# Performance work log

Measured on AMD Instinct MI355X. Metric: run time of the kernel, lower is better.

The kernel has to match this reference:

```python
import jax, jax.numpy as jnp
import numpy as np

T, B, C, H, W = 40, 256, 32, 8, 8
D = C * H * W  # 2048 flattened enc dim


def setup_inputs() -> dict:
    key = jax.random.key(0)
    k0, k1, k2 = jax.random.split(key, 3)
    x = jax.random.normal(k0, (T, B, C, H, W), dtype=jnp.float32)
    W0 = jax.random.normal(k1, (4 * C, 2 * C, 5, 5), dtype=jnp.float32) * 0.05
    b0 = jnp.zeros((4 * C,), dtype=jnp.float32)
    W1 = jax.random.normal(k2, (4 * C, 2 * C, 3, 3), dtype=jnp.float32) * 0.05
    b1 = jnp.zeros((4 * C,), dtype=jnp.float32)
    return {"x": x, "W0": W0, "b0": b0, "W1": W1, "b1": b1}


def _conv(x, w, b, pad):
    y = jax.lax.conv_general_dilated(
        x, w, window_strides=(1, 1), padding=[(pad, pad), (pad, pad)],
        dimension_numbers=("NCHW", "OIHW", "NCHW"))
    return y + b[None, :, None, None]


def _cell(inp, h, c, w, b, pad):
    # ConvLSTMCell: conv over concat(input, hidden) -> 4 gates
    g = _conv(jnp.concatenate([inp, h], axis=1), w, b, pad)
    i_g, f_g, o_g, c_g = jnp.split(g, 4, axis=1)
    c_new = jax.nn.sigmoid(f_g) * c + jax.nn.sigmoid(i_g) * jnp.tanh(c_g)
    h_new = jax.nn.sigmoid(o_g) * jnp.tanh(c_new)
    return h_new, c_new


def reference(x, W0, b0, W1, b1):
    Tn, Bn, Cn, Hn, Wn = x.shape
    Dn = Cn * Hn * Wn
    zeros = jnp.zeros((Bn, Cn, Hn, Wn), x.dtype)
    buf0 = jnp.zeros((Tn, Bn, Dn), x.dtype)  # growing prev_encs buffer, masked
    steps = jnp.arange(Tn)

    def body(carry, xt_t):
        xt, t = xt_t
        h0, c0, h1, c1, buf = carry
        h0, c0 = _cell(xt, h0, c0, W0, b0, 2)  # cell0: k=5, pad=2
        flat = h0.reshape(Bn, Dn)
        buf = buf.at[t].set(flat)
        # attention over encs[0..t] (softmax over a single entry at t=0 -> enc itself)
        dots = jnp.einsum("bd,tbd->bt", flat, buf)
        dots = jnp.where((steps <= t)[None, :], dots, -jnp.inf)
        wts = jax.nn.softmax(dots, axis=1)
        att = jnp.einsum("bt,tbd->bd", wts, buf).reshape(Bn, Cn, Hn, Wn)
        h1, c1 = _cell(att, h1, c1, W1, b1, 1)  # cell1: k=3, pad=1
        return (h0, c0, h1, c1, buf), h1

    _, ys = jax.lax.scan(body, (zeros, zeros, zeros, zeros, buf0), (x, steps))
    return ys  # [T, B, C, 8, 8]
```

## Files before the change

### kernel.cpp

```cpp
#include <hip/hip_runtime.h>

#define TT 40
#define NB 256
#define DD 2048
#define HISTL 28

typedef __bf16 bf16x8 __attribute__((ext_vector_type(8)));
typedef float f32x4 __attribute__((ext_vector_type(4)));
typedef unsigned short u16;
typedef unsigned int u32;
typedef u16 u16x8 __attribute__((ext_vector_type(8)));
typedef u16 u16x4 __attribute__((ext_vector_type(4)));

__device__ __forceinline__ u16 f2bf(float f) {
  u32 u = __builtin_bit_cast(u32, f);
  return (u16)((u + 0x7fffu + ((u >> 16) & 1u)) >> 16);
}
__device__ __forceinline__ float bf2f(u16 h) {
  return __builtin_bit_cast(float, ((u32)h) << 16);
}
__device__ __forceinline__ bf16x8 asbf(u16x8 v) { return __builtin_bit_cast(bf16x8, v); }

__device__ __forceinline__ float sigm(float x) { return 1.0f / (1.0f + __expf(-x)); }
__device__ __forceinline__ float tanh_(float x) {
  float e = __expf(-2.0f * fabsf(x));
  float t = (1.0f - e) / (1.0f + e);
  return copysignf(t, x);
}

__device__ __forceinline__ f32x4 mfma16(bf16x8 a, bf16x8 b, f32x4 c) {
  return __builtin_amdgcn_mfma_f32_16x16x32_bf16(a, b, c, 0, 0, 0);
}

__global__ void prep_weights(const float* __restrict__ W0, const float* __restrict__ W1,
                             u16* __restrict__ A0, u16* __restrict__ A1) {
  int tid = blockIdx.x * 256 + threadIdx.x;
  if (tid < 25600) {
    int lane = tid & 63;
    int kt = tid >> 9;
    int p = ((tid >> 6) & 7) * 16 + (lane & 15);
    int oc = (p & 3) * 32 + ((p >> 5) & 3) * 8 + ((p >> 4) & 1) * 4 + ((p >> 2) & 3);
    int kb = kt * 32 + (lane >> 4) * 8;
#pragma unroll
    for (int j = 0; j < 8; ++j) {
      int k = kb + j;
      int pos = k >> 6, ic = k & 63;
      int ky = pos / 5, kx = pos - ky * 5;
      A0[tid * 8 + j] = f2bf(W0[((oc * 64 + ic) * 5 + ky) * 5 + kx]);
    }
  } else if (tid < 25600 + 9216) {
    int t2 = tid - 25600;
    int lane = t2 & 63;
    int kt = t2 >> 9;
    int p = ((t2 >> 6) & 7) * 16 + (lane & 15);
    int oc = (p & 3) * 32 + ((p >> 5) & 3) * 8 + ((p >> 4) & 1) * 4 + ((p >> 2) & 3);
    int kb = kt * 32 + (lane >> 4) * 8;
#pragma unroll
    for (int j = 0; j < 8; ++j) {
      int k = kb + j;
      int pos = k >> 6, ic = k & 63;
      int ky = pos / 3, kx = pos - ky * 3;
      A1[t2 * 8 + j] = f2bf(W1[((oc * 64 + ic) * 3 + ky) * 3 + kx]);
    }
  }
}

template <int KK, int NKT, int SKB>
__device__ __forceinline__ void conv_loop(const u16* __restrict__ wsA, const u16* img,
                                          int w, int lane, f32x4 acc[4]) {
  const int ic0v = (lane >> 4) << 3;
  const int pb0 = ((lane & 15) >> 3) * 12 + (lane & 7);
  const bf16x8* A = (const bf16x8*)wsA;
  int aidx = w * 64 + lane;
  bf16x8 a0 = A[aidx];
  bf16x8 a1 = A[aidx + 512];
#pragma unroll
  for (int kt = 0; kt < NKT; ++kt) {
    bf16x8 nx = a1;
    if (kt + 2 < NKT) nx = A[aidx + 1024];
    const int pos = kt >> 1, ih = kt & 1;
    const int ky = pos / KK, kx = pos - ky * KK;
    const int Pb = pb0 + (ky * 12 + kx + SKB);
    const int idx = Pb * 64 + ((ic0v ^ ((Pb & 7) << 3)) ^ (ih << 5));
    u16x8 b0v = *(const u16x8*)(img + idx);
    u16x8 b1v = *(const u16x8*)(img + idx + 1536);
    u16x8 b2v = *(const u16x8*)(img + idx + 3072);
    u16x8 b3v = *(const u16x8*)(img + idx + 4608);
    acc[0] = mfma16(a0, asbf(b0v), acc[0]);
    acc[1] = mfma16(a0, asbf(b1v), acc[1]);
    acc[2] = mfma16(a0, asbf(b2v), acc[2]);
    acc[3] = mfma16(a0, asbf(b3v), acc[3]);
    a0 = a1;
    a1 = nx;
    aidx += 512;
  }
}

__device__ __forceinline__ int imin(int a, int b) { return a < b ? a : b; }

__global__ void __launch_bounds__(512, 1)
convlstm_main(const float* __restrict__ x, const float* __restrict__ b0g,
              const float* __restrict__ b1g, const u16* __restrict__ wsA0,
              const u16* __restrict__ wsA1, u16* __restrict__ buf,
              float* __restrict__ out) {
  alignas(16) __shared__ u16 imgA[9216];
  alignas(16) __shared__ u16 imgB[9216];
  alignas(16) __shared__ u16 hist[HISTL * DD];
  alignas(16) __shared__ u16 curr[DD];
  __shared__ float sdots[64];
  __shared__ float swts[64];

  const int tid = threadIdx.x;
  const int b = blockIdx.x;
  const int lane = tid & 63;
  const int w = tid >> 6;
  const int h = lane >> 4;
  const int l15 = lane & 15;

  for (int i = tid; i < 9216; i += 512) {
    imgA[i] = 0;
    imgB[i] = 0;
  }

  float c0st[4] = {};
  float c1st[4] = {};
  float bi0[4], bi1[4];
  const int ch = ((w >> 1) & 3) * 8 + (w & 1) * 4 + h;
#pragma unroll
  for (int j = 0; j < 4; ++j) {
    bi0[j] = b0g[j * 32 + ch];
    bi1[j] = b1g[j * 32 + ch];
  }

  const int Pldx = ((lane >> 3) + 2) * 12 + (lane & 7) + 2;
  const int swx = (Pldx & 7) << 3;
  const int Pl0 = ((l15 >> 3) + 2) * 12 + (l15 & 7) + 2;
  const int swh = (Pl0 & 7) << 3;
  const int e4 = tid * 4;
  const int chAtt = tid >> 4;
  const int pix0 = (tid & 15) * 4;
  const int PaB = ((pix0 >> 3) + 2) * 12 + (pix0 & 7) + 2;

  float xr[4];
  {
    const float* xp = x + (size_t)b * DD;
#pragma unroll
    for (int i = 0; i < 4; ++i) xr[i] = xp[(i * 8 + w) * 64 + lane];
  }

  __syncthreads();

  for (int t = 0; t < TT; ++t) {
#pragma unroll
    for (int i = 0; i < 4; ++i) {
      int c = i * 8 + w;
      imgA[Pldx * 64 + (c ^ swx)] = f2bf(xr[i]);
    }
    __syncthreads();

    if (t + 1 < TT) {
      const float* xp = x + (size_t)((t + 1) * NB + b) * DD;
#pragma unroll
      for (int i = 0; i < 4; ++i) xr[i] = xp[(i * 8 + w) * 64 + lane];
    }

    f32x4 acc[4];
    f32x4 zz = {0.f, 0.f, 0.f, 0.f};
#pragma unroll
    for (int nt = 0; nt < 4; ++nt) acc[nt] = zz;
    conv_loop<5, 50, 0>(wsA0, imgA, w, lane, acc);
    __syncthreads();

    u16* bufrow = buf + (size_t)(t * NB + b) * DD;
#pragma unroll
    for (int nt = 0; nt < 4; ++nt) {
      float ig = acc[nt][0] + bi0[0];
      float fg = acc[nt][1] + bi0[1];
      float og = acc[nt][2] + bi0[2];
      float cg = acc[nt][3] + bi0[3];
      float cn = sigm(fg) * c0st[nt] + sigm(ig) * tanh_(cg);
      float hn = sigm(og) * tanh_(cn);
      c0st[nt] = cn;
      u16 hb = f2bf(hn);
      imgA[(Pl0 + 24 * nt) * 64 + ((32 + ch) ^ swh)] = hb;
      int d = ch * 64 + nt * 16 + l15;
      curr[d] = hb;
      if (t < HISTL)
        hist[t * DD + d] = hb;
      else
        bufrow[d] = hb;
    }
    __syncthreads();

    {
      u16x8 fv[4];
      {
        const u16x8* rowT = (const u16x8*)curr;
#pragma unroll
        for (int i = 0; i < 4; ++i) fv[i] = rowT[i * 64 + lane];
      }
      int tp = w;
      for (; tp <= t && tp < HISTL; tp += 8) {
        const u16x8* rowP = (const u16x8*)&hist[tp * DD];
        u16x8 p0 = rowP[lane], p1 = rowP[64 + lane], p2 = rowP[128 + lane], p3 = rowP[192 + lane];
        float s0 = 0.f, s1 = 0.f, s2 = 0.f, s3 = 0.f;
#pragma unroll
        for (int j = 0; j < 8; ++j) {
          s0 += bf2f(fv[0][j]) * bf2f(p0[j]);
          s1 += bf2f(fv[1][j]) * bf2f(p1[j]);
          s2 += bf2f(fv[2][j]) * bf2f(p2[j]);
          s3 += bf2f(fv[3][j]) * bf2f(p3[j]);
        }
        float s = (s0 + s1) + (s2 + s3);
#pragma unroll
        for (int off = 32; off; off >>= 1) s += __shfl_xor(s, off, 64);
        if (lane == 0) sdots[tp] = s;
      }
      for (; tp < t; tp += 8) {
        const u16x8* rowP = (const u16x8*)(buf + (size_t)(tp * NB + b) * DD);
        u16x8 p0 = rowP[lane], p1 = rowP[64 + lane], p2 = rowP[128 + lane], p3 = rowP[192 + lane];
        float s0 = 0.f, s1 = 0.f, s2 = 0.f, s3 = 0.f;
#pragma unroll
        for (int j = 0; j < 8; ++j) {
          s0 += bf2f(fv[0][j]) * bf2f(p0[j]);
          s1 += bf2f(fv[1][j]) * bf2f(p1[j]);
          s2 += bf2f(fv[2][j]) * bf2f(p2[j]);
          s3 += bf2f(fv[3][j]) * bf2f(p3[j]);
        }
        float s = (s0 + s1) + (s2 + s3);
#pragma unroll
        for (int off = 32; off; off >>= 1) s += __shfl_xor(s, off, 64);
        if (lane == 0) sdots[tp] = s;
      }
      if (tp == t) {
        float s0 = 0.f, s1 = 0.f, s2 = 0.f, s3 = 0.f;
#pragma unroll
        for (int j = 0; j < 8; ++j) {
          s0 += bf2f(fv[0][j]) * bf2f(fv[0][j]);
          s1 += bf2f(fv[1][j]) * bf2f(fv[1][j]);
          s2 += bf2f(fv[2][j]) * bf2f(fv[2][j]);
          s3 += bf2f(fv[3][j]) * bf2f(fv[3][j]);
        }
        float s = (s0 + s1) + (s2 + s3);
#pragma unroll
        for (int off = 32; off; off >>= 1) s += __shfl_xor(s, off, 64);
        if (lane == 0) sdots[tp] = s;
      }
    }
    __syncthreads();

    if (w == 0) {
      float v = (lane <= t) ? sdots[lane] : -3.0e38f;
      float m = v;
#pragma unroll
      for (int off = 32; off; off >>= 1) m = fmaxf(m, __shfl_xor(m, off, 64));
      float e = (lane <= t) ? __expf(v - m) : 0.f;
      float ss = e;
#pragma unroll
      for (int off = 32; off; off >>= 1) ss += __shfl_xor(ss, off, 64);
      swts[lane] = e / ss;
    }
    __syncthreads();

    {
      float av0 = 0.f, av1 = 0.f, av2 = 0.f, av3 = 0.f;
      const int lim = imin(t, HISTL);
      int tp = 0;
      for (; tp + 1 < lim; tp += 2) {
        float wa = swts[tp], wb = swts[tp + 1];
        u16x4 va = *(const u16x4*)&hist[tp * DD + e4];
        u16x4 vb = *(const u16x4*)&hist[(tp + 1) * DD + e4];
        av0 = fmaf(wa, bf2f(va[0]), av0);
        av1 = fmaf(wa, bf2f(va[1]), av1);
        av2 = fmaf(wa, bf2f(va[2]), av2);
        av3 = fmaf(wa, bf2f(va[3]), av3);
        av0 = fmaf(wb, bf2f(vb[0]), av0);
        av1 = fmaf(wb, bf2f(vb[1]), av1);
        av2 = fmaf(wb, bf2f(vb[2]), av2);
        av3 = fmaf(wb, bf2f(vb[3]), av3);
      }
      if (tp < lim) {
        float wa = swts[tp];
        u16x4 va = *(const u16x4*)&hist[tp * DD + e4];
        av0 = fmaf(wa, bf2f(va[0]), av0);
        av1 = fmaf(wa, bf2f(va[1]), av1);
        av2 = fmaf(wa, bf2f(va[2]), av2);
        av3 = fmaf(wa, bf2f(va[3]), av3);
      }
      tp = HISTL;
      for (; tp + 1 < t; tp += 2) {
        float wa = swts[tp], wb = swts[tp + 1];
        u16x4 va = *(const u16x4*)(buf + (size_t)(tp * NB + b) * DD + e4);
        u16x4 vb = *(const u16x4*)(buf + (size_t)((tp + 1) * NB + b) * DD + e4);
        av0 = fmaf(wa, bf2f(va[0]), av0);
        av1 = fmaf(wa, bf2f(va[1]), av1);
        av2 = fmaf(wa, bf2f(va[2]), av2);
        av3 = fmaf(wa, bf2f(va[3]), av3);
        av0 = fmaf(wb, bf2f(vb[0]), av0);
        av1 = fmaf(wb, bf2f(vb[1]), av1);
        av2 = fmaf(wb, bf2f(vb[2]), av2);
        av3 = fmaf(wb, bf2f(vb[3]), av3);
      }
      if (tp < t) {
        float wa = swts[tp];
        u16x4 va = *(const u16x4*)(buf + (size_t)(tp * NB + b) * DD + e4);
        av0 = fmaf(wa, bf2f(va[0]), av0);
        av1 = fmaf(wa, bf2f(va[1]), av1);
        av2 = fmaf(wa, bf2f(va[2]), av2);
        av3 = fmaf(wa, bf2f(va[3]), av3);
      }
      {
        float wa = swts[t];
        u16x4 va = *(const u16x4*)&curr[e4];
        av0 = fmaf(wa, bf2f(va[0]), av0);
        av1 = fmaf(wa, bf2f(va[1]), av1);
        av2 = fmaf(wa, bf2f(va[2]), av2);
        av3 = fmaf(wa, bf2f(va[3]), av3);
      }
      float av[4] = {av0, av1, av2, av3};
#pragma unroll
      for (int j = 0; j < 4; ++j) {
        int P = PaB + j;
        imgB[P * 64 + (chAtt ^ ((P & 7) << 3))] = f2bf(av[j]);
      }
    }
    __syncthreads();

#pragma unroll
    for (int nt = 0; nt < 4; ++nt) acc[nt] = zz;
    conv_loop<3, 18, 13>(wsA1, imgB, w, lane, acc);
    __syncthreads();

    float* outrow = out + (size_t)(t * NB + b) * DD;
#pragma unroll
    for (int nt = 0; nt < 4; ++nt) {
      float ig = acc[nt][0] + bi1[0];
      float fg = acc[nt][1] + bi1[1];
      float og = acc[nt][2] + bi1[2];
      float cg = acc[nt][3] + bi1[3];
      float cn = sigm(fg) * c1st[nt] + sigm(ig) * tanh_(cg);
      float hn = sigm(og) * tanh_(cn);
      c1st[nt] = cn;
      imgB[(Pl0 + 24 * nt) * 64 + ((32 + ch) ^ swh)] = f2bf(hn);
      outrow[ch * 64 + nt * 16 + l15] = hn;
    }
    __syncthreads();
  }
}

extern "C" void kernel_launch(void* const* d_in, const int* in_sizes, int n_in,
                              void* d_out, int out_size, void* d_ws, size_t ws_size,
                              hipStream_t stream) {
  const float* x = (const float*)d_in[0];
  const float* W0 = (const float*)d_in[1];
  const float* b0 = (const float*)d_in[2];
  const float* W1 = (const float*)d_in[3];
  const float* b1 = (const float*)d_in[4];
  float* out = (float*)d_out;

  u16* A0 = (u16*)d_ws;
  u16* A1 = A0 + 204800;
  u16* buf = (u16*)((char*)d_ws + (1 << 20));

  prep_weights<<<136, 256, 0, stream>>>(W0, W1, A0, A1);
  convlstm_main<<<256, 512, 0, stream>>>(x, b0, b1, A0, A1, buf, out);
}
```

Before: 1.491 ms.

## Cut per-step barriers by deferring smem writes and replicating softmax per wave

```diff
diff --git a/kernel.cpp b/kernel.cpp
--- a/kernel.cpp
+++ b/kernel.cpp
@@ -74,10 +74,12 @@
   int aidx = w * 64 + lane;
   bf16x8 a0 = A[aidx];
   bf16x8 a1 = A[aidx + 512];
+  bf16x8 a2 = A[aidx + 1024];
+  bf16x8 a3 = A[aidx + 1536];
 #pragma unroll
   for (int kt = 0; kt < NKT; ++kt) {
-    bf16x8 nx = a1;
-    if (kt + 2 < NKT) nx = A[aidx + 1024];
+    bf16x8 nx = a3;
+    if (kt + 4 < NKT) nx = A[aidx + 2048];
     const int pos = kt >> 1, ih = kt & 1;
     const int ky = pos / KK, kx = pos - ky * KK;
     const int Pb = pb0 + (ky * 12 + kx + SKB);
@@ -91,7 +93,9 @@
     acc[2] = mfma16(a0, asbf(b2v), acc[2]);
     acc[3] = mfma16(a0, asbf(b3v), acc[3]);
     a0 = a1;
-    a1 = nx;
+    a1 = a2;
+    a2 = a3;
+    a3 = nx;
     aidx += 512;
   }
 }
@@ -108,7 +112,6 @@
   alignas(16) __shared__ u16 hist[HISTL * DD];
   alignas(16) __shared__ u16 curr[DD];
   __shared__ float sdots[64];
-  __shared__ float swts[64];
 
   const int tid = threadIdx.x;
   const int b = blockIdx.x;
@@ -143,33 +146,29 @@
 
   float xr[4];
   {
-    const float* xp = x + (size_t)b * DD;
-#pragma unroll
-    for (int i = 0; i < 4; ++i) xr[i] = xp[(i * 8 + w) * 64 + lane];
-  }
-
-  __syncthreads();
-
-  for (int t = 0; t < TT; ++t) {
+    const float* xp0 = x + (size_t)b * DD;
 #pragma unroll
     for (int i = 0; i < 4; ++i) {
       int c = i * 8 + w;
-      imgA[Pldx * 64 + (c ^ swx)] = f2bf(xr[i]);
-    }
-    __syncthreads();
-
-    if (t + 1 < TT) {
-      const float* xp = x + (size_t)((t + 1) * NB + b) * DD;
-#pragma unroll
-      for (int i = 0; i < 4; ++i) xr[i] = xp[(i * 8 + w) * 64 + lane];
-    }
-
+      imgA[Pldx * 64 + (c ^ swx)] = f2bf(__builtin_nontemporal_load(xp0 + c * 64 + lane));
+    }
+    const float* xp1 = x + (size_t)(NB + b) * DD;
+#pragma unroll
+    for (int i = 0; i < 4; ++i)
+      xr[i] = __builtin_nontemporal_load(xp1 + (i * 8 + w) * 64 + lane);
+  }
+
+  u16 hb[4];
+  u16 h1b[4];
+
+  __syncthreads();
+
+  for (int t = 0; t < TT; ++t) {
     f32x4 acc[4];
     f32x4 zz = {0.f, 0.f, 0.f, 0.f};
 #pragma unroll
     for (int nt = 0; nt < 4; ++nt) acc[nt] = zz;
     conv_loop<5, 50, 0>(wsA0, imgA, w, lane, acc);
-    __syncthreads();
 
     u16* bufrow = buf + (size_t)(t * NB + b) * DD;
 #pragma unroll
@@ -181,16 +180,38 @@
       float cn = sigm(fg) * c0st[nt] + sigm(ig) * tanh_(cg);
       float hn = sigm(og) * tanh_(cn);
       c0st[nt] = cn;
-      u16 hb = f2bf(hn);
-      imgA[(Pl0 + 24 * nt) * 64 + ((32 + ch) ^ swh)] = hb;
+      u16 hv = f2bf(hn);
+      hb[nt] = hv;
       int d = ch * 64 + nt * 16 + l15;
-      curr[d] = hb;
+      curr[d] = hv;
       if (t < HISTL)
-        hist[t * DD + d] = hb;
+        hist[t * DD + d] = hv;
       else
-        bufrow[d] = hb;
+        bufrow[d] = hv;
     }
     __syncthreads();
+
+#pragma unroll
+    for (int nt = 0; nt < 4; ++nt)
+      imgA[(Pl0 + 24 * nt) * 64 + ((32 + ch) ^ swh)] = hb[nt];
+    if (t > 0) {
+#pragma unroll
+      for (int nt = 0; nt < 4; ++nt)
+        imgB[(Pl0 + 24 * nt) * 64 + ((32 + ch) ^ swh)] = h1b[nt];
+    }
+    if (t + 1 < TT) {
+#pragma unroll
+      for (int i = 0; i < 4; ++i) {
+        int c = i * 8 + w;
+        imgA[Pldx * 64 + (c ^ swx)] = f2bf(xr[i]);
+      }
+    }
+    if (t + 2 < TT) {
+      const float* xp = x + (size_t)((t + 2) * NB + b) * DD;
+#pragma unroll
+      for (int i = 0; i < 4; ++i)
+        xr[i] = __builtin_nontemporal_load(xp + (i * 8 + w) * 64 + lane);
+    }
 
     {
       u16x8 fv[4];
@@ -249,7 +270,8 @@
     }
     __syncthreads();
 
-    if (w == 0) {
+    float myw;
+    {
       float v = (lane <= t) ? sdots[lane] : -3.0e38f;
       float m = v;
 #pragma unroll
@@ -258,16 +280,15 @@
       float ss = e;
 #pragma unroll
       for (int off = 32; off; off >>= 1) ss += __shfl_xor(ss, off, 64);
-      swts[lane] = e / ss;
-    }
-    __syncthreads();
+      myw = e / ss;
+    }
 
     {
       float av0 = 0.f, av1 = 0.f, av2 = 0.f, av3 = 0.f;
       const int lim = imin(t, HISTL);
       int tp = 0;
       for (; tp + 1 < lim; tp += 2) {
-        float wa = swts[tp], wb = swts[tp + 1];
+        float wa = __shfl(myw, tp, 64), wb = __shfl(myw, tp + 1, 64);
         u16x4 va = *(const u16x4*)&hist[tp * DD + e4];
         u16x4 vb = *(const u16x4*)&hist[(tp + 1) * DD + e4];
         av0 = fmaf(wa, bf2f(va[0]), av0);
@@ -280,7 +301,7 @@
         av3 = fmaf(wb, bf2f(vb[3]), av3);
       }
       if (tp < lim) {
-        float wa = swts[tp];
+        float wa = __shfl(myw, tp, 64);
         u16x4 va = *(const u16x4*)&hist[tp * DD + e4];
         av0 = fmaf(wa, bf2f(va[0]), av0);
         av1 = fmaf(wa, bf2f(va[1]), av1);
@@ -289,7 +310,7 @@
       }
       tp = HISTL;
       for (; tp + 1 < t; tp += 2) {
-        float wa = swts[tp], wb = swts[tp + 1];
+        float wa = __shfl(myw, tp, 64), wb = __shfl(myw, tp + 1, 64);
         u16x4 va = *(const u16x4*)(buf + (size_t)(tp * NB + b) * DD + e4);
         u16x4 vb = *(const u16x4*)(buf + (size_t)((tp + 1) * NB + b) * DD + e4);
         av0 = fmaf(wa, bf2f(va[0]), av0);
@@ -302,7 +323,7 @@
         av3 = fmaf(wb, bf2f(vb[3]), av3);
       }
       if (tp < t) {
-        float wa = swts[tp];
+        float wa = __shfl(myw, tp, 64);
         u16x4 va = *(const u16x4*)(buf + (size_t)(tp * NB + b) * DD + e4);
         av0 = fmaf(wa, bf2f(va[0]), av0);
         av1 = fmaf(wa, bf2f(va[1]), av1);
@@ -310,7 +331,7 @@
         av3 = fmaf(wa, bf2f(va[3]), av3);
       }
       {
-        float wa = swts[t];
+        float wa = __shfl(myw, t, 64);
         u16x4 va = *(const u16x4*)&curr[e4];
         av0 = fmaf(wa, bf2f(va[0]), av0);
         av1 = fmaf(wa, bf2f(va[1]), av1);
@@ -329,7 +350,6 @@
 #pragma unroll
     for (int nt = 0; nt < 4; ++nt) acc[nt] = zz;
     conv_loop<3, 18, 13>(wsA1, imgB, w, lane, acc);
-    __syncthreads();
 
     float* outrow = out + (size_t)(t * NB + b) * DD;
 #pragma unroll
@@ -341,10 +361,9 @@
       float cn = sigm(fg) * c1st[nt] + sigm(ig) * tanh_(cg);
       float hn = sigm(og) * tanh_(cn);
       c1st[nt] = cn;
-      imgB[(Pl0 + 24 * nt) * 64 + ((32 + ch) ^ swh)] = f2bf(hn);
-      outrow[ch * 64 + nt * 16 + l15] = hn;
-    }
-    __syncthreads();
+      h1b[nt] = f2bf(hn);
+      __builtin_nontemporal_store(hn, outrow + ch * 64 + nt * 16 + l15);
+    }
   }
 }
 
```

Result: faster. 1.424 ms (-4.5%).
